# Performance work log

Hardware: AMD Instinct MI355X
Metric: run time of the kernel (lower is better)

## Reference

```python
import jax, jax.numpy as jnp
import numpy as np

B, R, N, D_IN, D_OUT = 8, 4, 1024, 256, 256


def setup_inputs() -> dict:
    key = jax.random.key(0)
    k1, k2, k3, k4 = jax.random.split(key, 4)
    text = jax.random.normal(k1, (B, N, D_IN), dtype=jnp.float32)
    adj = jax.random.uniform(k2, (B, R, N, N), dtype=jnp.float32)
    weight = jax.random.normal(k3, (R, D_IN, D_OUT), dtype=jnp.float32) * 0.02
    bias = jax.random.normal(k4, (D_OUT,), dtype=jnp.float32) * 0.02
    return {"text": text, "adj": adj, "weight": weight, "bias": bias}


def reference(text, adj, weight, bias):
    # Row-normalize adjacency per relation (diag_embed+matmul in torch == row scale).
    rowsum = adj.sum(axis=-1)                                   # [B,R,N]
    r_inv = jnp.where(rowsum == 0, 0.0, 1.0 / rowsum)           # inf -> 0
    norm_adj = adj * r_inv[..., None]                           # [B,R,N,N]
    # Per-relation message passing, batched over relations.
    hidden = jnp.einsum('brij,bjd->brid', norm_adj, text)       # [B,R,N,D_in]
    # Concat over relations along feature dim: [B,N,R*D_in]
    tmp = jnp.transpose(hidden, (0, 2, 1, 3)).reshape(text.shape[0], text.shape[1], -1)
    w = weight.reshape(-1, weight.shape[-1])                    # [R*D_in, D_out]
    return tmp @ w + bias
```

## Files before the change

kernel.cpp:

```cpp
#include <hip/hip_runtime.h>
#include <hip/hip_bf16.h>
#include <hip/hip_fp16.h>
#include <stdint.h>

typedef __bf16 bf16_8 __attribute__((ext_vector_type(8)));
typedef float f32x4 __attribute__((ext_vector_type(4)));
typedef unsigned int u32;
typedef unsigned short u16;


__device__ __forceinline__ u16 f2b(float f) {
    return __builtin_bit_cast(u16, __float2bfloat16(f));
}
__device__ __forceinline__ u16 f2h(float f) {
    return __builtin_bit_cast(u16, __float2half(f));
}

__device__ __forceinline__ u32 swz_off(u32 row, u32 g) {
    return (row * 4u + (g ^ ((row >> 1) & 3u))) * 16u;
}

__device__ __forceinline__ void gload_lds16(const void* g, void* l) {
    __builtin_amdgcn_global_load_lds((const __attribute__((address_space(1))) void*)g,
                                     (__attribute__((address_space(3))) void*)l, 16, 0, 0);
}

__device__ __forceinline__ void memfence_sched() { asm volatile("" ::: "memory"); }

__device__ __forceinline__ uint4 pack8(float4 a, float4 b) {
    uint4 pk;
    pk.x = (u32)f2b(a.x) | ((u32)f2b(a.y) << 16);
    pk.y = (u32)f2b(a.z) | ((u32)f2b(a.w) << 16);
    pk.z = (u32)f2b(b.x) | ((u32)f2b(b.y) << 16);
    pk.w = (u32)f2b(b.z) | ((u32)f2b(b.w) << 16);
    return pk;
}

__global__ __launch_bounds__(256) void prep_cvt_kernel(const float* text, u16* textb,
                                                       const float* W, u16* Wt) {
    const u32 bid = blockIdx.x;
    if (bid < 1024u) {
        const u32 i8 = bid * 256u + threadIdx.x;
        const float4 a = ((const float4*)text)[i8 * 2u];
        const float4 b = ((const float4*)text)[i8 * 2u + 1u];
        ((uint4*)textb)[i8] = pack8(a, b);
    } else {
        const u32 idx = (bid - 1024u) * 256u + threadIdx.x;
        const u32 r = idx >> 16, rem = idx & 65535u, dout = rem >> 8, din = rem & 255u;
        Wt[idx] = f2b(W[(r << 16) + (din << 8) + dout]);
    }
}

__global__ __launch_bounds__(256) void y_gemm_kernel(const u16* Wt, const u16* textb,
                                                     u16* Yt) {
    __shared__ char smem[49152];
    char* bufA = smem;
    char* bufB = smem + 24576;

    const u32 bx = blockIdx.x;
    const u32 n0 = (bx & 7u) * 128u;
    const u32 m0 = ((bx >> 3) & 1u) * 128u;
    const u32 r  = (bx >> 4) & 3u;
    const u32 b  = bx >> 6;
    const u16* pA = Wt + (size_t)r * 65536u + (size_t)m0 * 256u;
    const u16* pB = textb + (size_t)b * 262144u + (size_t)n0 * 256u;

    const u32 t    = threadIdx.x;
    const u32 lane = t & 63u;
    const u32 w    = t >> 6;
    const u32 wm   = (w >> 1) * 64u;
    const u32 wn   = (w & 1u) * 64u;
    const u32 waveByte = (t & 192u) * 16u;
    const u32 row0 = t >> 2;
    const u32 gg0  = (t & 3u) ^ ((row0 >> 1) & 3u);
    const u32 row1 = row0 + 64u;
    const u32 gg1  = ((t + 256u) & 3u) ^ ((row1 >> 1) & 3u);
    const u32 fr = lane & 15u;
    const u32 fg = lane >> 4;

    const u16* a0p = pA + (size_t)row0 * 256u + gg0 * 8u;
    const u16* a1p = pA + (size_t)row1 * 256u + gg1 * 8u;
    const u16* b0p = pB + (size_t)row0 * 256u + gg0 * 8u;
    const u16* b1p = pB + (size_t)row1 * 256u + gg1 * 8u;

    f32x4 acc[4][4];
#pragma unroll
    for (int i = 0; i < 4; ++i)
#pragma unroll
        for (int j = 0; j < 4; ++j) acc[i][j] = (f32x4){0.f, 0.f, 0.f, 0.f};

    auto stage = [&](u32 ks, u32 slot) {
        const u32 k0 = ks * 32u;
        gload_lds16(a0p + k0, bufA + slot * 8192u + waveByte);
        gload_lds16(a1p + k0, bufA + slot * 8192u + waveByte + 4096u);
        gload_lds16(b0p + k0, bufB + slot * 8192u + waveByte);
        gload_lds16(b1p + k0, bufB + slot * 8192u + waveByte + 4096u);
    };
    auto do_mfma = [&](u32 slot) {
        char* curA = bufA + slot * 8192u;
        char* curB = bufB + slot * 8192u;
        bf16_8 af[4], bfv[4];
#pragma unroll
        for (int mt = 0; mt < 4; ++mt) {
            uint4 v = *(const uint4*)(curA + swz_off(wm + (u32)mt * 16u + fr, fg));
            af[mt] = __builtin_bit_cast(bf16_8, v);
        }
#pragma unroll
        for (int nt = 0; nt < 4; ++nt) {
            uint4 v = *(const uint4*)(curB + swz_off(wn + (u32)nt * 16u + fr, fg));
            bfv[nt] = __builtin_bit_cast(bf16_8, v);
        }
#pragma unroll
        for (int mt = 0; mt < 4; ++mt)
#pragma unroll
            for (int nt = 0; nt < 4; ++nt)
                acc[mt][nt] = __builtin_amdgcn_mfma_f32_16x16x32_bf16(af[mt], bfv[nt],
                                                                      acc[mt][nt], 0, 0, 0);
    };

    stage(0u, 0u);
    memfence_sched();
    stage(1u, 1u);
    memfence_sched();
    asm volatile("s_waitcnt vmcnt(4)" ::: "memory");
    __builtin_amdgcn_s_barrier();

#pragma unroll 6
    for (int ks = 0; ks < 6; ++ks) {
        stage((u32)(ks + 2), (u32)((ks + 2) % 3));
        memfence_sched();
        do_mfma((u32)(ks % 3));
        asm volatile("s_waitcnt vmcnt(4) lgkmcnt(0)" ::: "memory");
        __builtin_amdgcn_s_barrier();
    }
    do_mfma(0u);
    asm volatile("s_waitcnt vmcnt(0) lgkmcnt(0)" ::: "memory");
    __builtin_amdgcn_s_barrier();
    do_mfma(1u);

    const u32 rit = fg * 4u, cit = fr;
    u16* yb = Yt + (size_t)(b * 4u + r) * 262144u;
#pragma unroll
    for (int mt = 0; mt < 4; ++mt)
#pragma unroll
        for (int nt = 0; nt < 4; ++nt) {
            const u32 m = m0 + wm + (u32)mt * 16u + rit;
            const u32 n = n0 + wn + (u32)nt * 16u + cit;
#pragma unroll
            for (int rg = 0; rg < 4; ++rg)
                yb[(size_t)(m + (u32)rg) * 1024u + n] = f2b(acc[mt][nt][rg]);
        }
}

__global__ __launch_bounds__(512, 2) void adj_gemm_partial(const float* adj,
                                                           const u16* Yt,
                                                           u16* partial) {
    __shared__ char smem[66048];
    char* bufA = smem;
    char* bufB = smem + 16384;
    float* sInv = (float*)(smem + 65536);

    const u32 raw = blockIdx.x;
    const u32 bx = (raw & 7u) * 32u + (raw >> 3);
    const u32 i0 = (bx & 7u) * 128u;
    const u32 r  = (bx >> 3) & 3u;
    const u32 b  = bx >> 5;

    const float* pA = adj + (((size_t)(b * 4u + r)) << 20) + (size_t)i0 * 1024u;
    const u16*   pB = Yt + (((size_t)(b * 4u + r)) << 18);

    const u32 t = threadIdx.x, lane = t & 63u, w = t >> 6;
    const u32 wm = (w >> 2) * 64u;
    const u32 wn = (w & 3u) * 64u;
    const u32 fr = lane & 15u, fg = lane >> 4;

    const u32 sRow = t >> 2;
    const u32 cSwz = (t & 3u) ^ ((sRow >> 1) & 3u);
    const float* aSrc = pA + (size_t)sRow * 1024u + cSwz * 8u;

    const u32 brow0 = t >> 2;
    const u32 brow1 = (t + 512u) >> 2;
    const u32 bg0 = (t & 3u) ^ ((brow0 >> 1) & 3u);
    const u32 bg1 = (t & 3u) ^ ((brow1 >> 1) & 3u);
    const u16* b0p = pB + (size_t)brow0 * 1024u + bg0 * 8u;
    const u16* b1p = pB + (size_t)brow1 * 1024u + bg1 * 8u;
    const u32 waveB = (t & 448u) * 16u;

    f32x4 acc[4][4];
#pragma unroll
    for (int i = 0; i < 4; ++i)
#pragma unroll
        for (int j = 0; j < 4; ++j) acc[i][j] = (f32x4){0.f, 0.f, 0.f, 0.f};

    float s0 = 0.f;
    float4 rA[2][2];

    auto loadA = [&](float4* dst, u32 kt) {
        dst[0] = *(const float4*)(aSrc + kt * 32u);
        dst[1] = *(const float4*)(aSrc + kt * 32u + 4u);
    };
    auto stageB = [&](u32 kt, char* dst) {
        gload_lds16(b0p + kt * 32u, dst + waveB);
        gload_lds16(b1p + kt * 32u, dst + 8192u + waveB);
    };
    auto packA = [&](const float4* a2, char* dst) {
        s0 += (a2[0].x + a2[0].y + a2[0].z + a2[0].w)
            + (a2[1].x + a2[1].y + a2[1].z + a2[1].w);
        *(uint4*)(dst + t * 16u) = pack8(a2[0], a2[1]);
    };
    auto do_mfma = [&](char* curA, char* curB) {
        bf16_8 af[4], bfv[4];
#pragma unroll
        for (int mt = 0; mt < 4; ++mt) {
            uint4 v = *(const uint4*)(curA + swz_off(wm + (u32)mt * 16u + fr, fg));
            af[mt] = __builtin_bit_cast(bf16_8, v);
        }
#pragma unroll
        for (int nt = 0; nt < 4; ++nt) {
            uint4 v = *(const uint4*)(curB + swz_off(wn + (u32)nt * 16u + fr, fg));
            bfv[nt] = __builtin_bit_cast(bf16_8, v);
        }
#pragma unroll
        for (int mt = 0; mt < 4; ++mt)
#pragma unroll
            for (int nt = 0; nt < 4; ++nt)
                acc[mt][nt] = __builtin_amdgcn_mfma_f32_16x16x32_bf16(af[mt], bfv[nt],
                                                                      acc[mt][nt], 0, 0, 0);
    };

    loadA(rA[0], 0u);
    stageB(0u, bufB);
    memfence_sched();
    loadA(rA[1], 1u);
    stageB(1u, bufB + 16384u);
    memfence_sched();
    packA(rA[0], bufA);
    asm volatile("s_waitcnt vmcnt(4) lgkmcnt(0)" ::: "memory");
    __builtin_amdgcn_s_barrier();

#pragma unroll 6
    for (int ks = 0; ks < 30; ++ks) {
        const u32 cA = (u32)ks & 1u, nA = cA ^ 1u;
        packA(rA[nA], bufA + nA * 8192u);
        loadA(rA[cA], (u32)(ks + 2));
        stageB((u32)(ks + 2), bufB + (u32)((ks + 2) % 3) * 16384u);
        do_mfma(bufA + cA * 8192u, bufB + (u32)(ks % 3) * 16384u);
        asm volatile("s_waitcnt vmcnt(4) lgkmcnt(0)" ::: "memory");
        __builtin_amdgcn_s_barrier();
    }
    packA(rA[1], bufA + 8192u);
    do_mfma(bufA, bufB);
    asm volatile("s_waitcnt vmcnt(0) lgkmcnt(0)" ::: "memory");
    __builtin_amdgcn_s_barrier();
    do_mfma(bufA + 8192u, bufB + 16384u);

    s0 += __shfl_down(s0, 2, 64);
    s0 += __shfl_down(s0, 1, 64);
    if ((t & 3u) == 0u) sInv[sRow] = (s0 == 0.f) ? 0.f : 1.f / s0;
    __syncthreads();

    u16* pp = partial + (((size_t)(b * 4u + r)) << 18) + (size_t)i0 * 256u;
#pragma unroll
    for (int mt = 0; mt < 4; ++mt)
#pragma unroll
        for (int rg = 0; rg < 4; ++rg) {
            const u32 mRow = wm + (u32)mt * 16u + fg * 4u + (u32)rg;
            const float inv = sInv[mRow];
#pragma unroll
            for (int nt = 0; nt < 4; ++nt)
                pp[(size_t)mRow * 256u + wn + (u32)nt * 16u + fr] =
                    f2h(acc[mt][nt][rg] * inv);
        }
}

__global__ __launch_bounds__(256) void reduce_kernel(const u16* partial,
                                                     const float* bias, float* out) {
    const u32 i8 = blockIdx.x * 256u + threadIdx.x;
    const u32 b = i8 >> 15;
    const u32 rem8 = (i8 & 32767u) * 8u;
    const u32 d0 = rem8 & 255u;

    const float4 bv0 = *(const float4*)(bias + d0);
    const float4 bv1 = *(const float4*)(bias + d0 + 4u);
    float s[8] = {bv0.x, bv0.y, bv0.z, bv0.w, bv1.x, bv1.y, bv1.z, bv1.w};

#pragma unroll
    for (u32 r = 0; r < 4u; ++r) {
        const uint4 v = *(const uint4*)(partial + (((size_t)(b * 4u + r)) << 18) + rem8);
        const u16* h = (const u16*)&v;
#pragma unroll
        for (int j = 0; j < 8; ++j)
            s[j] += __half2float(__builtin_bit_cast(__half, h[j]));
    }
    const float4 o0 = {s[0], s[1], s[2], s[3]};
    const float4 o1 = {s[4], s[5], s[6], s[7]};
    ((float4*)out)[i8 * 2u] = o0;
    ((float4*)out)[i8 * 2u + 1u] = o1;
}

extern "C" void kernel_launch(void* const* d_in, const int* in_sizes, int n_in,
                              void* d_out, int out_size, void* d_ws, size_t ws_size,
                              hipStream_t stream) {
    const float* text = (const float*)d_in[0];
    const float* adj  = (const float*)d_in[1];
    const float* wgt  = (const float*)d_in[2];
    const float* bias = (const float*)d_in[3];
    float* out = (float*)d_out;

    char* ws = (char*)d_ws;
    u16* Yt      = (u16*)ws;
    u16* textb   = (u16*)(ws + 16777216u);
    u16* Wt      = (u16*)(ws + 20971520u);
    u16* partial = (u16*)(ws + 21495808u);

    prep_cvt_kernel<<<2048, 256, 0, stream>>>(text, textb, wgt, Wt);
    y_gemm_kernel<<<512, 256, 0, stream>>>(Wt, textb, Yt);
    adj_gemm_partial<<<256, 512, 0, stream>>>(adj, Yt, partial);
    reduce_kernel<<<1024, 256, 0, stream>>>(partial, bias, out);
}
```

Measured before the change: 59.55 us.

## Fuse text fp32-to-bf16 conversion into Y GEMM B-operand loading

Drops the separate text conversion pass: the Y GEMM now loads fp32 text straight into registers, packs it to bf16 and writes it into a double-buffered LDS tile, while A still uses direct global-to-LDS loads. This removes the write and re-read of the bf16 text copy, and the weight transpose now runs as its own smaller kernel. The block index is also remapped to change the order in which tiles are scheduled. The cost is more global bytes per B tile (fp32), extra registers and VALU packing work inside the main loop, and more complex wait counts.

```diff
diff --git a/kernel.cpp b/kernel.cpp
--- a/kernel.cpp
+++ b/kernel.cpp
@@ -36,34 +36,26 @@
     return pk;
 }
 
-__global__ __launch_bounds__(256) void prep_cvt_kernel(const float* text, u16* textb,
-                                                       const float* W, u16* Wt) {
-    const u32 bid = blockIdx.x;
-    if (bid < 1024u) {
-        const u32 i8 = bid * 256u + threadIdx.x;
-        const float4 a = ((const float4*)text)[i8 * 2u];
-        const float4 b = ((const float4*)text)[i8 * 2u + 1u];
-        ((uint4*)textb)[i8] = pack8(a, b);
-    } else {
-        const u32 idx = (bid - 1024u) * 256u + threadIdx.x;
-        const u32 r = idx >> 16, rem = idx & 65535u, dout = rem >> 8, din = rem & 255u;
-        Wt[idx] = f2b(W[(r << 16) + (din << 8) + dout]);
-    }
-}
-
-__global__ __launch_bounds__(256) void y_gemm_kernel(const u16* Wt, const u16* textb,
+__global__ __launch_bounds__(256) void wt_cvt_kernel(const float* W, u16* Wt) {
+    const u32 idx = blockIdx.x * 256u + threadIdx.x;
+    const u32 r = idx >> 16, rem = idx & 65535u, dout = rem >> 8, din = rem & 255u;
+    Wt[idx] = f2b(W[(r << 16) + (din << 8) + dout]);
+}
+
+__global__ __launch_bounds__(256) void y_gemm_kernel(const u16* Wt, const float* text,
                                                      u16* Yt) {
-    __shared__ char smem[49152];
+    __shared__ char smem[40960];
     char* bufA = smem;
     char* bufB = smem + 24576;
 
-    const u32 bx = blockIdx.x;
+    const u32 raw = blockIdx.x;
+    const u32 bx = (raw & 7u) * 64u + (raw >> 3);
     const u32 n0 = (bx & 7u) * 128u;
     const u32 m0 = ((bx >> 3) & 1u) * 128u;
     const u32 r  = (bx >> 4) & 3u;
     const u32 b  = bx >> 6;
     const u16* pA = Wt + (size_t)r * 65536u + (size_t)m0 * 256u;
-    const u16* pB = textb + (size_t)b * 262144u + (size_t)n0 * 256u;
+    const float* pT = text + (size_t)b * 262144u + (size_t)n0 * 256u;
 
     const u32 t    = threadIdx.x;
     const u32 lane = t & 63u;
@@ -71,17 +63,22 @@
     const u32 wm   = (w >> 1) * 64u;
     const u32 wn   = (w & 1u) * 64u;
     const u32 waveByte = (t & 192u) * 16u;
-    const u32 row0 = t >> 2;
-    const u32 gg0  = (t & 3u) ^ ((row0 >> 1) & 3u);
-    const u32 row1 = row0 + 64u;
-    const u32 gg1  = ((t + 256u) & 3u) ^ ((row1 >> 1) & 3u);
     const u32 fr = lane & 15u;
     const u32 fg = lane >> 4;
 
-    const u16* a0p = pA + (size_t)row0 * 256u + gg0 * 8u;
-    const u16* a1p = pA + (size_t)row1 * 256u + gg1 * 8u;
-    const u16* b0p = pB + (size_t)row0 * 256u + gg0 * 8u;
-    const u16* b1p = pB + (size_t)row1 * 256u + gg1 * 8u;
+    const u32 arow0 = t >> 2;
+    const u32 agg0  = (t & 3u) ^ ((arow0 >> 1) & 3u);
+    const u32 arow1 = arow0 + 64u;
+    const u32 agg1  = ((t + 256u) & 3u) ^ ((arow1 >> 1) & 3u);
+    const u16* a0p = pA + (size_t)arow0 * 256u + agg0 * 8u;
+    const u16* a1p = pA + (size_t)arow1 * 256u + agg1 * 8u;
+
+    const u32 brow0 = t >> 2;
+    const u32 bc    = t & 3u;
+    const u32 bsw0  = (brow0 >> 1) & 3u;
+    const u32 bsw1  = ((brow0 + 64u) >> 1) & 3u;
+    const float* bSrc0 = pT + (size_t)brow0 * 256u + (bc ^ bsw0) * 8u;
+    const float* bSrc1 = pT + (size_t)(brow0 + 64u) * 256u + (bc ^ bsw1) * 8u;
 
     f32x4 acc[4][4];
 #pragma unroll
@@ -89,16 +86,25 @@
 #pragma unroll
         for (int j = 0; j < 4; ++j) acc[i][j] = (f32x4){0.f, 0.f, 0.f, 0.f};
 
-    auto stage = [&](u32 ks, u32 slot) {
-        const u32 k0 = ks * 32u;
-        gload_lds16(a0p + k0, bufA + slot * 8192u + waveByte);
-        gload_lds16(a1p + k0, bufA + slot * 8192u + waveByte + 4096u);
-        gload_lds16(b0p + k0, bufB + slot * 8192u + waveByte);
-        gload_lds16(b1p + k0, bufB + slot * 8192u + waveByte + 4096u);
-    };
-    auto do_mfma = [&](u32 slot) {
-        char* curA = bufA + slot * 8192u;
-        char* curB = bufB + slot * 8192u;
+    float4 rB[2][4];
+
+    auto loadB = [&](float4* dst, u32 kt) {
+        dst[0] = *(const float4*)(bSrc0 + kt * 32u);
+        dst[1] = *(const float4*)(bSrc0 + kt * 32u + 4u);
+        dst[2] = *(const float4*)(bSrc1 + kt * 32u);
+        dst[3] = *(const float4*)(bSrc1 + kt * 32u + 4u);
+    };
+    auto stageA = [&](u32 kt, u32 slot) {
+        gload_lds16(a0p + kt * 32u, bufA + slot * 8192u + waveByte);
+        gload_lds16(a1p + kt * 32u, bufA + slot * 8192u + waveByte + 4096u);
+    };
+    auto packB = [&](const float4* rs, char* dst) {
+        *(uint4*)(dst + t * 16u) = pack8(rs[0], rs[1]);
+        *(uint4*)(dst + 4096u + t * 16u) = pack8(rs[2], rs[3]);
+    };
+    auto do_mfma = [&](u32 slotA, u32 slotB) {
+        char* curA = bufA + slotA * 8192u;
+        char* curB = bufB + slotB * 8192u;
         bf16_8 af[4], bfv[4];
 #pragma unroll
         for (int mt = 0; mt < 4; ++mt) {
@@ -118,25 +124,31 @@
                                                                       acc[mt][nt], 0, 0, 0);
     };
 
-    stage(0u, 0u);
+    loadB(rB[0], 0u);
+    stageA(0u, 0u);
     memfence_sched();
-    stage(1u, 1u);
+    loadB(rB[1], 1u);
+    stageA(1u, 1u);
     memfence_sched();
-    asm volatile("s_waitcnt vmcnt(4)" ::: "memory");
+    packB(rB[0], bufB);
+    asm volatile("s_waitcnt vmcnt(6) lgkmcnt(0)" ::: "memory");
     __builtin_amdgcn_s_barrier();
 
 #pragma unroll 6
     for (int ks = 0; ks < 6; ++ks) {
-        stage((u32)(ks + 2), (u32)((ks + 2) % 3));
-        memfence_sched();
-        do_mfma((u32)(ks % 3));
-        asm volatile("s_waitcnt vmcnt(4) lgkmcnt(0)" ::: "memory");
+        const u32 cB = (u32)ks & 1u, nB = cB ^ 1u;
+        packB(rB[nB], bufB + nB * 8192u);
+        loadB(rB[cB], (u32)(ks + 2));
+        stageA((u32)(ks + 2), (u32)((ks + 2) % 3));
+        do_mfma((u32)(ks % 3), cB);
+        asm volatile("s_waitcnt vmcnt(6) lgkmcnt(0)" ::: "memory");
         __builtin_amdgcn_s_barrier();
     }
-    do_mfma(0u);
+    packB(rB[1], bufB + 8192u);
+    do_mfma(0u, 0u);
     asm volatile("s_waitcnt vmcnt(0) lgkmcnt(0)" ::: "memory");
     __builtin_amdgcn_s_barrier();
-    do_mfma(1u);
+    do_mfma(1u, 1u);
 
     const u32 rit = fg * 4u, cit = fr;
     u16* yb = Yt + (size_t)(b * 4u + r) * 262144u;
@@ -309,12 +321,11 @@
 
     char* ws = (char*)d_ws;
     u16* Yt      = (u16*)ws;
-    u16* textb   = (u16*)(ws + 16777216u);
-    u16* Wt      = (u16*)(ws + 20971520u);
-    u16* partial = (u16*)(ws + 21495808u);
-
-    prep_cvt_kernel<<<2048, 256, 0, stream>>>(text, textb, wgt, Wt);
-    y_gemm_kernel<<<512, 256, 0, stream>>>(Wt, textb, Yt);
+    u16* Wt      = (u16*)(ws + 16777216u);
+    u16* partial = (u16*)(ws + 17301504u);
+
+    wt_cvt_kernel<<<1024, 256, 0, stream>>>(wgt, Wt);
+    y_gemm_kernel<<<512, 256, 0, stream>>>(Wt, text, Yt);
     adj_gemm_partial<<<256, 512, 0, stream>>>(adj, Yt, partial);
     reduce_kernel<<<1024, 256, 0, stream>>>(partial, bias, out);
 }
```

Result: slower. 62.26 us (+4.6%).
